# Kernel optimization log

Hardware: AMD Instinct MI355X
Metric: run time of the kernel (lower is better)

The kernel has to match this reference:

```python
import jax, jax.numpy as jnp
import numpy as np

N_NODES = 50000
N_EDGES = 600000
D = 128


def setup_inputs() -> dict:
    key = jax.random.key(0)
    k1, k2, k3, k4, k5, k6 = jax.random.split(key, 6)
    x = jax.random.normal(k1, (N_NODES, D), dtype=jnp.float32)
    edge_index = jax.random.randint(k2, (2, N_EDGES), 0, N_NODES, dtype=jnp.int64)
    # nn.Linear default init: U(-1/sqrt(fan_in), 1/sqrt(fan_in))
    bound = 1.0 / np.sqrt(D)
    W1 = jax.random.uniform(k3, (D, D), minval=-bound, maxval=bound, dtype=jnp.float32)
    b1 = jax.random.uniform(k4, (D,), minval=-bound, maxval=bound, dtype=jnp.float32)
    W2 = jax.random.uniform(k5, (D, D), minval=-bound, maxval=bound, dtype=jnp.float32)
    b2 = jax.random.uniform(k6, (D,), minval=-bound, maxval=bound, dtype=jnp.float32)
    return {"x": x, "edge_index": edge_index, "W1": W1, "b1": b1, "W2": W2, "b2": b2}


def reference(x, edge_index, W1, b1, W2, b2):
    row, col = edge_index[0], edge_index[1]
    n = x.shape[0]
    # degree of each node as aggregation target, clamped to >= 1
    deg = jax.ops.segment_sum(jnp.ones(row.shape, dtype=x.dtype), row, num_segments=n)
    deg = jnp.maximum(deg, 1.0)[:, None]  # [N, 1]
    # round 1: gather neighbors, scatter-add by row, normalize, linear+relu
    agg = jax.ops.segment_sum(x[col], row, num_segments=n)  # [N, D]
    h = jax.nn.relu((agg / deg) @ W1.T + b1)
    # round 2
    agg2 = jax.ops.segment_sum(h[col], row, num_segments=n)  # [N, D]
    return jax.nn.relu((agg2 / deg) @ W2.T + b2)
```

## Files before the change

### kernel.cpp

```cpp
#include <hip/hip_runtime.h>
#include <hip/hip_fp16.h>

#define D 128
#define TILE_R 64

typedef _Float16 h8 __attribute__((ext_vector_type(8)));
typedef float f4 __attribute__((ext_vector_type(4)));

__global__ __launch_bounds__(256) void prep_kernel(const float* __restrict__ in,
                                                   __half* __restrict__ out, int n8,
                                                   int* __restrict__ hist, int n,
                                                   const float* __restrict__ W1,
                                                   __half* __restrict__ WB1,
                                                   const float* __restrict__ W2,
                                                   __half* __restrict__ WB2) {
    if (blockIdx.x < 2) {
        const float* W = blockIdx.x ? W2 : W1;
        __half* WB     = blockIdx.x ? WB2 : WB1;
        for (int idx = threadIdx.x; idx < D * D; idx += 256) {
            int j  = idx & 7;
            int l  = (idx >> 3) & 63;
            int kk = (idx >> 9) & 3;
            int c  = idx >> 11;
            int k   = kk * 32 + (l >> 4) * 8 + j;
            int col = c * 16 + (l & 15);
            WB[idx] = __float2half(W[col * D + k]);
        }
        return;
    }
    int i = (blockIdx.x - 2) * 256 + threadIdx.x;
    if (i < n) hist[i] = 0;
    if (i >= n8) return;
    float4 a = ((const float4*)in)[2 * i];
    float4 b = ((const float4*)in)[2 * i + 1];
    __half2 h[4];
    h[0] = __float22half2_rn(make_float2(a.x, a.y));
    h[1] = __float22half2_rn(make_float2(a.z, a.w));
    h[2] = __float22half2_rn(make_float2(b.x, b.y));
    h[3] = __float22half2_rn(make_float2(b.z, b.w));
    ((float4*)out)[i] = *(const float4*)h;
}

__global__ __launch_bounds__(256) void hist_kernel(const int* __restrict__ row,
                                                   int* __restrict__ hist, int e) {
    int i = blockIdx.x * blockDim.x + threadIdx.x;
    if (i < e) atomicAdd(&hist[row[i]], 1);
}

__global__ __launch_bounds__(256) void partial_kernel(const int* __restrict__ hist,
                                                      int* __restrict__ bsum, int n) {
    int i = blockIdx.x * 256 + threadIdx.x;
    int v = (i < n) ? hist[i] : 0;
#pragma unroll
    for (int off = 1; off < 64; off <<= 1) v += __shfl_xor(v, off);
    __shared__ int ws[4];
    int lane = threadIdx.x & 63, w = threadIdx.x >> 6;
    if (lane == 0) ws[w] = v;
    __syncthreads();
    if (threadIdx.x == 0) bsum[blockIdx.x] = ws[0] + ws[1] + ws[2] + ws[3];
}

__global__ __launch_bounds__(256) void finalize_kernel(const int* __restrict__ hist,
                                                       const int* __restrict__ bsum,
                                                       int* __restrict__ offsets,
                                                       int* __restrict__ cursor,
                                                       float* __restrict__ rdeg, int n) {
    __shared__ int wt[4];
    int t = threadIdx.x, lane = t & 63, w = t >> 6;

    int p = 0;
    for (int k = t; k < blockIdx.x; k += 256) p += bsum[k];
#pragma unroll
    for (int off = 1; off < 64; off <<= 1) p += __shfl_xor(p, off);
    if (lane == 0) wt[w] = p;
    __syncthreads();
    int blockbase = wt[0] + wt[1] + wt[2] + wt[3];
    __syncthreads();

    int i = blockIdx.x * 256 + t;
    int v = (i < n) ? hist[i] : 0;
    int iv = v;
#pragma unroll
    for (int off = 1; off < 64; off <<= 1) {
        int n2 = __shfl_up(iv, off);
        if (lane >= off) iv += n2;
    }
    if (lane == 63) wt[w] = iv;
    __syncthreads();
    int add = blockbase;
    for (int k = 0; k < w; ++k) add += wt[k];
    int excl = iv - v + add;
    if (i < n) {
        offsets[i] = excl;
        cursor[i]  = excl;
        rdeg[i]    = 1.0f / fmaxf((float)v, 1.0f);
    }
}

__global__ __launch_bounds__(256) void fill_kernel(const int* __restrict__ ei, int e,
                                                   int* __restrict__ cursor,
                                                   int* __restrict__ csr) {
    int i = blockIdx.x * blockDim.x + threadIdx.x;
    if (i < e) {
        int r = ei[i];
        int c = ei[e + i];
        int pos = atomicAdd(&cursor[r], 1);
        csr[pos] = c;
    }
}

__global__ __launch_bounds__(256) void linear_kernel(const __half* __restrict__ src,
                                                     const __half* __restrict__ WB,
                                                     __half* __restrict__ z, int n) {
    alignas(16) __shared__ __half Bs[D * D];
    {
        const float4* wb4 = (const float4*)WB;
        float4* bs4 = (float4*)Bs;
        for (int i = threadIdx.x; i < D * D / 8; i += 256) bs4[i] = wb4[i];
    }
    __syncthreads();

    int l    = threadIdx.x & 63;
    int wv   = threadIdx.x >> 6;
    int row0 = blockIdx.x * TILE_R + wv * 16;
    int arow = row0 + (l & 15);
    bool rowok = arow < n;

    h8 a[4];
#pragma unroll
    for (int kk = 0; kk < 4; ++kk) {
        if (rowok)
            a[kk] = *(const h8*)&src[(size_t)arow * D + kk * 32 + (l >> 4) * 8];
        else
            a[kk] = (h8)(_Float16)0.0f;
    }

    int srow = row0 + (l >> 4) * 4;
#pragma unroll
    for (int c = 0; c < 8; ++c) {
        f4 acc = {0.f, 0.f, 0.f, 0.f};
#pragma unroll
        for (int kk = 0; kk < 4; ++kk) {
            h8 b = *(const h8*)&Bs[(((c * 4 + kk) * 64) + l) * 8];
            acc = __builtin_amdgcn_mfma_f32_16x16x32_f16(a[kk], b, acc, 0, 0, 0);
        }
        int col = c * 16 + (l & 15);
#pragma unroll
        for (int r = 0; r < 4; ++r) {
            int ro = srow + r;
            if (ro < n) z[(size_t)ro * D + col] = __float2half(acc[r]);
        }
    }
}

__device__ inline void addh8(float* a, float4 v) {
    const __half2* h = (const __half2*)&v;
    float2 f0 = __half22float2(h[0]);
    float2 f1 = __half22float2(h[1]);
    float2 f2 = __half22float2(h[2]);
    float2 f3 = __half22float2(h[3]);
    a[0] += f0.x; a[1] += f0.y; a[2] += f1.x; a[3] += f1.y;
    a[4] += f2.x; a[5] += f2.y; a[6] += f3.x; a[7] += f3.y;
}

template <int OUT_HALF>
__global__ __launch_bounds__(256) void gather_kernel(const __half* __restrict__ z,
                                                     const int* __restrict__ offsets,
                                                     const int* __restrict__ hist,
                                                     const int* __restrict__ csr,
                                                     const float* __restrict__ rdeg,
                                                     const float* __restrict__ bias,
                                                     void* __restrict__ outv, int n) {
    int tid  = blockIdx.x * 256 + threadIdx.x;
    int wave = tid >> 6;
    int lane = threadIdx.x & 63;
    int g    = lane >> 4;
    int gl   = lane & 15;
    int node = wave * 4 + g;
    if (node >= n) return;

    int start = offsets[node];
    int cnt   = hist[node];
    const float4* base = (const float4*)z;

    float acc[8] = {0.f, 0.f, 0.f, 0.f, 0.f, 0.f, 0.f, 0.f};
    int i = 0;
    for (; i + 8 <= cnt; i += 8) {
        int c0 = csr[start + i];
        int c1 = csr[start + i + 1];
        int c2 = csr[start + i + 2];
        int c3 = csr[start + i + 3];
        int c4 = csr[start + i + 4];
        int c5 = csr[start + i + 5];
        int c6 = csr[start + i + 6];
        int c7 = csr[start + i + 7];
        float4 v0 = base[(size_t)c0 * 16 + gl];
        float4 v1 = base[(size_t)c1 * 16 + gl];
        float4 v2 = base[(size_t)c2 * 16 + gl];
        float4 v3 = base[(size_t)c3 * 16 + gl];
        float4 v4 = base[(size_t)c4 * 16 + gl];
        float4 v5 = base[(size_t)c5 * 16 + gl];
        float4 v6 = base[(size_t)c6 * 16 + gl];
        float4 v7 = base[(size_t)c7 * 16 + gl];
        addh8(acc, v0); addh8(acc, v1); addh8(acc, v2); addh8(acc, v3);
        addh8(acc, v4); addh8(acc, v5); addh8(acc, v6); addh8(acc, v7);
    }
    if (i + 4 <= cnt) {
        int c0 = csr[start + i];
        int c1 = csr[start + i + 1];
        int c2 = csr[start + i + 2];
        int c3 = csr[start + i + 3];
        float4 v0 = base[(size_t)c0 * 16 + gl];
        float4 v1 = base[(size_t)c1 * 16 + gl];
        float4 v2 = base[(size_t)c2 * 16 + gl];
        float4 v3 = base[(size_t)c3 * 16 + gl];
        addh8(acc, v0); addh8(acc, v1); addh8(acc, v2); addh8(acc, v3);
        i += 4;
    }
    int rem = cnt - i;
    if (rem > 0) {
        int c0 = csr[start + i];
        int c1 = csr[start + min(i + 1, cnt - 1)];
        int c2 = csr[start + min(i + 2, cnt - 1)];
        float4 v0 = base[(size_t)c0 * 16 + gl];
        float4 v1 = base[(size_t)c1 * 16 + gl];
        float4 v2 = base[(size_t)c2 * 16 + gl];
        addh8(acc, v0);
        if (rem > 1) addh8(acc, v1);
        if (rem > 2) addh8(acc, v2);
    }

    float rd = rdeg[node];
    float4 b0 = ((const float4*)bias)[gl * 2];
    float4 b1 = ((const float4*)bias)[gl * 2 + 1];
    float o[8];
    o[0] = fmaxf(acc[0] * rd + b0.x, 0.f);
    o[1] = fmaxf(acc[1] * rd + b0.y, 0.f);
    o[2] = fmaxf(acc[2] * rd + b0.z, 0.f);
    o[3] = fmaxf(acc[3] * rd + b0.w, 0.f);
    o[4] = fmaxf(acc[4] * rd + b1.x, 0.f);
    o[5] = fmaxf(acc[5] * rd + b1.y, 0.f);
    o[6] = fmaxf(acc[6] * rd + b1.z, 0.f);
    o[7] = fmaxf(acc[7] * rd + b1.w, 0.f);

    if (OUT_HALF) {
        __half2 h[4];
        h[0] = __float22half2_rn(make_float2(o[0], o[1]));
        h[1] = __float22half2_rn(make_float2(o[2], o[3]));
        h[2] = __float22half2_rn(make_float2(o[4], o[5]));
        h[3] = __float22half2_rn(make_float2(o[6], o[7]));
        ((float4*)outv)[(size_t)node * 16 + gl] = *(const float4*)h;
    } else {
        float4* o4 = (float4*)outv;
        o4[(size_t)node * 32 + gl * 2]     = make_float4(o[0], o[1], o[2], o[3]);
        o4[(size_t)node * 32 + gl * 2 + 1] = make_float4(o[4], o[5], o[6], o[7]);
    }
}

extern "C" void kernel_launch(void* const* d_in, const int* in_sizes, int n_in,
                              void* d_out, int out_size, void* d_ws, size_t ws_size,
                              hipStream_t stream) {
    const float* x  = (const float*)d_in[0];
    const int*   ei = (const int*)d_in[1];
    const float* W1 = (const float*)d_in[2];
    const float* b1 = (const float*)d_in[3];
    const float* W2 = (const float*)d_in[4];
    const float* b2 = (const float*)d_in[5];
    float* out = (float*)d_out;

    int N = in_sizes[0] / D;
    int E = in_sizes[1] / 2;
    int NB = (N + 255) / 256;

    int* hist    = (int*)d_ws;
    int* offsets = hist + N;
    int* cursor  = offsets + N;
    int* csr     = cursor + N;
    float* rdeg  = (float*)(csr + E);
    int* bsum    = (int*)(rdeg + N);
    __half* WB1  = (__half*)(bsum + ((NB + 3) & ~3));
    __half* WB2  = WB1 + D * D;
    __half* xh   = WB2 + D * D;
    __half* hh   = xh + (size_t)N * D;
    __half* zz   = hh + (size_t)N * D;

    prep_kernel<<<(N * D / 8 + 255) / 256 + 2, 256, 0, stream>>>(x, xh, N * D / 8, hist, N,
                                                                 W1, WB1, W2, WB2);
    hist_kernel<<<(E + 255) / 256, 256, 0, stream>>>(ei, hist, E);
    partial_kernel<<<NB, 256, 0, stream>>>(hist, bsum, N);
    finalize_kernel<<<NB, 256, 0, stream>>>(hist, bsum, offsets, cursor, rdeg, N);
    fill_kernel<<<(E + 255) / 256, 256, 0, stream>>>(ei, E, cursor, csr);

    int nblk = (N + TILE_R - 1) / TILE_R;
    int gblk = ((N + 3) / 4 * 64 + 255) / 256;
    linear_kernel<<<nblk, 256, 0, stream>>>(xh, WB1, zz, N);
    gather_kernel<1><<<gblk, 256, 0, stream>>>(zz, offsets, hist, csr, rdeg, b1, hh, N);
    linear_kernel<<<nblk, 256, 0, stream>>>(hh, WB2, zz, N);
    gather_kernel<0><<<gblk, 256, 0, stream>>>(zz, offsets, hist, csr, rdeg, b2, out, N);
}
```

Baseline: 167.1 us.

## Fuse fp32-to-fp16 cast into first linear, merge fill with linear, drop partial scan

Removes the separate x-to-half conversion pass by converting fp32 rows directly while loading MFMA fragments in the first linear. The CSR fill and the first linear are launched as one kernel with disjoint block ranges so they can run concurrently. The partial-sum kernel is removed, and each finalize block instead sums all preceding hist entries directly. That costs redundant O(N) reads per block, up to about 50k ints for late blocks, in exchange for one fewer launch.

```diff
diff --git a/kernel.cpp b/kernel.cpp
--- a/kernel.cpp
+++ b/kernel.cpp
@@ -7,9 +7,7 @@
 typedef _Float16 h8 __attribute__((ext_vector_type(8)));
 typedef float f4 __attribute__((ext_vector_type(4)));
 
-__global__ __launch_bounds__(256) void prep_kernel(const float* __restrict__ in,
-                                                   __half* __restrict__ out, int n8,
-                                                   int* __restrict__ hist, int n,
+__global__ __launch_bounds__(256) void prep_kernel(int* __restrict__ hist, int n,
                                                    const float* __restrict__ W1,
                                                    __half* __restrict__ WB1,
                                                    const float* __restrict__ W2,
@@ -30,15 +28,6 @@
     }
     int i = (blockIdx.x - 2) * 256 + threadIdx.x;
     if (i < n) hist[i] = 0;
-    if (i >= n8) return;
-    float4 a = ((const float4*)in)[2 * i];
-    float4 b = ((const float4*)in)[2 * i + 1];
-    __half2 h[4];
-    h[0] = __float22half2_rn(make_float2(a.x, a.y));
-    h[1] = __float22half2_rn(make_float2(a.z, a.w));
-    h[2] = __float22half2_rn(make_float2(b.x, b.y));
-    h[3] = __float22half2_rn(make_float2(b.z, b.w));
-    ((float4*)out)[i] = *(const float4*)h;
 }
 
 __global__ __launch_bounds__(256) void hist_kernel(const int* __restrict__ row,
@@ -47,29 +36,16 @@
     if (i < e) atomicAdd(&hist[row[i]], 1);
 }
 
-__global__ __launch_bounds__(256) void partial_kernel(const int* __restrict__ hist,
-                                                      int* __restrict__ bsum, int n) {
-    int i = blockIdx.x * 256 + threadIdx.x;
-    int v = (i < n) ? hist[i] : 0;
-#pragma unroll
-    for (int off = 1; off < 64; off <<= 1) v += __shfl_xor(v, off);
-    __shared__ int ws[4];
-    int lane = threadIdx.x & 63, w = threadIdx.x >> 6;
-    if (lane == 0) ws[w] = v;
-    __syncthreads();
-    if (threadIdx.x == 0) bsum[blockIdx.x] = ws[0] + ws[1] + ws[2] + ws[3];
-}
-
 __global__ __launch_bounds__(256) void finalize_kernel(const int* __restrict__ hist,
-                                                       const int* __restrict__ bsum,
                                                        int* __restrict__ offsets,
                                                        int* __restrict__ cursor,
                                                        float* __restrict__ rdeg, int n) {
     __shared__ int wt[4];
     int t = threadIdx.x, lane = t & 63, w = t >> 6;
 
+    int limit = blockIdx.x * 256;
     int p = 0;
-    for (int k = t; k < blockIdx.x; k += 256) p += bsum[k];
+    for (int k = t; k < limit; k += 256) p += hist[k];
 #pragma unroll
     for (int off = 1; off < 64; off <<= 1) p += __shfl_xor(p, off);
     if (lane == 0) wt[w] = p;
@@ -77,7 +53,7 @@
     int blockbase = wt[0] + wt[1] + wt[2] + wt[3];
     __syncthreads();
 
-    int i = blockIdx.x * 256 + t;
+    int i = limit + t;
     int v = (i < n) ? hist[i] : 0;
     int iv = v;
 #pragma unroll
@@ -97,21 +73,20 @@
     }
 }
 
-__global__ __launch_bounds__(256) void fill_kernel(const int* __restrict__ ei, int e,
-                                                   int* __restrict__ cursor,
-                                                   int* __restrict__ csr) {
-    int i = blockIdx.x * blockDim.x + threadIdx.x;
-    if (i < e) {
-        int r = ei[i];
-        int c = ei[e + i];
-        int pos = atomicAdd(&cursor[r], 1);
-        csr[pos] = c;
-    }
-}
-
-__global__ __launch_bounds__(256) void linear_kernel(const __half* __restrict__ src,
-                                                     const __half* __restrict__ WB,
-                                                     __half* __restrict__ z, int n) {
+__device__ inline h8 load_frag(const __half* p) { return *(const h8*)p; }
+__device__ inline h8 load_frag(const float* p) {
+    float4 u = *(const float4*)p;
+    float4 v = *(const float4*)(p + 4);
+    h8 r;
+    r[0] = (_Float16)u.x; r[1] = (_Float16)u.y; r[2] = (_Float16)u.z; r[3] = (_Float16)u.w;
+    r[4] = (_Float16)v.x; r[5] = (_Float16)v.y; r[6] = (_Float16)v.z; r[7] = (_Float16)v.w;
+    return r;
+}
+
+template <typename T>
+__device__ inline void linear_body(const T* __restrict__ src,
+                                   const __half* __restrict__ WB,
+                                   __half* __restrict__ z, int n, int blk) {
     alignas(16) __shared__ __half Bs[D * D];
     {
         const float4* wb4 = (const float4*)WB;
@@ -122,7 +97,7 @@
 
     int l    = threadIdx.x & 63;
     int wv   = threadIdx.x >> 6;
-    int row0 = blockIdx.x * TILE_R + wv * 16;
+    int row0 = blk * TILE_R + wv * 16;
     int arow = row0 + (l & 15);
     bool rowok = arow < n;
 
@@ -130,7 +105,7 @@
 #pragma unroll
     for (int kk = 0; kk < 4; ++kk) {
         if (rowok)
-            a[kk] = *(const h8*)&src[(size_t)arow * D + kk * 32 + (l >> 4) * 8];
+            a[kk] = load_frag(&src[(size_t)arow * D + kk * 32 + (l >> 4) * 8]);
         else
             a[kk] = (h8)(_Float16)0.0f;
     }
@@ -151,6 +126,31 @@
             if (ro < n) z[(size_t)ro * D + col] = __float2half(acc[r]);
         }
     }
+}
+
+__global__ __launch_bounds__(256) void fill_linear_kernel(const int* __restrict__ ei, int e,
+                                                          int* __restrict__ cursor,
+                                                          int* __restrict__ csr, int nfill,
+                                                          const float* __restrict__ x,
+                                                          const __half* __restrict__ WB,
+                                                          __half* __restrict__ z, int n) {
+    if (blockIdx.x < nfill) {
+        int i = blockIdx.x * 256 + threadIdx.x;
+        if (i < e) {
+            int r = ei[i];
+            int c = ei[e + i];
+            int pos = atomicAdd(&cursor[r], 1);
+            csr[pos] = c;
+        }
+        return;
+    }
+    linear_body<float>(x, WB, z, n, blockIdx.x - nfill);
+}
+
+__global__ __launch_bounds__(256) void linear_kernel(const __half* __restrict__ src,
+                                                     const __half* __restrict__ WB,
+                                                     __half* __restrict__ z, int n) {
+    linear_body<__half>(src, WB, z, n, blockIdx.x);
 }
 
 __device__ inline void addh8(float* a, float4 v) {
@@ -277,23 +277,21 @@
     int* cursor  = offsets + N;
     int* csr     = cursor + N;
     float* rdeg  = (float*)(csr + E);
-    int* bsum    = (int*)(rdeg + N);
-    __half* WB1  = (__half*)(bsum + ((NB + 3) & ~3));
+    __half* WB1  = (__half*)(rdeg + N);
     __half* WB2  = WB1 + D * D;
-    __half* xh   = WB2 + D * D;
-    __half* hh   = xh + (size_t)N * D;
+    __half* hh   = WB2 + D * D;
     __half* zz   = hh + (size_t)N * D;
 
-    prep_kernel<<<(N * D / 8 + 255) / 256 + 2, 256, 0, stream>>>(x, xh, N * D / 8, hist, N,
-                                                                 W1, WB1, W2, WB2);
+    prep_kernel<<<NB + 2, 256, 0, stream>>>(hist, N, W1, WB1, W2, WB2);
     hist_kernel<<<(E + 255) / 256, 256, 0, stream>>>(ei, hist, E);
-    partial_kernel<<<NB, 256, 0, stream>>>(hist, bsum, N);
-    finalize_kernel<<<NB, 256, 0, stream>>>(hist, bsum, offsets, cursor, rdeg, N);
-    fill_kernel<<<(E + 255) / 256, 256, 0, stream>>>(ei, E, cursor, csr);
-
-    int nblk = (N + TILE_R - 1) / TILE_R;
-    int gblk = ((N + 3) / 4 * 64 + 255) / 256;
-    linear_kernel<<<nblk, 256, 0, stream>>>(xh, WB1, zz, N);
+    finalize_kernel<<<NB, 256, 0, stream>>>(hist, offsets, cursor, rdeg, N);
+
+    int nblk  = (N + TILE_R - 1) / TILE_R;
+    int nfill = (E + 255) / 256;
+    int gblk  = ((N + 3) / 4 * 64 + 255) / 256;
+
+    fill_linear_kernel<<<nfill + nblk, 256, 0, stream>>>(ei, E, cursor, csr, nfill,
+                                                         x, WB1, zz, N);
     gather_kernel<1><<<gblk, 256, 0, stream>>>(zz, offsets, hist, csr, rdeg, b1, hh, N);
     linear_kernel<<<nblk, 256, 0, stream>>>(hh, WB2, zz, N);
     gather_kernel<0><<<gblk, 256, 0, stream>>>(zz, offsets, hist, csr, rdeg, b2, out, N);
```

New measurement: 175.4 us. +4.9%, slower.
